# Optimization experiments

Measured on AMD Instinct MI355X. Metric: run time of the kernel, lower is better.

Reference implementation:

```python
import jax, jax.numpy as jnp
import numpy as np

B, N, M, D = 4, 512, 512, 128
H, DOUT = 256, 128

def setup_inputs() -> dict:
    key = jax.random.key(0)
    k = jax.random.split(key, 4)
    X = jax.random.normal(k[0], (B, N, D), dtype=jnp.float32)
    Y = jax.random.normal(k[1], (B, M, D), dtype=jnp.float32)
    W1 = jax.random.normal(k[2], (2 * D, H), dtype=jnp.float32) / np.sqrt(2 * D)
    b1 = jnp.zeros((H,), dtype=jnp.float32)
    W2 = jax.random.normal(k[3], (H, DOUT), dtype=jnp.float32) / np.sqrt(H)
    b2 = jnp.zeros((DOUT,), dtype=jnp.float32)
    return {"X": X, "Y": Y, "W1": W1, "b1": b1, "W2": W2, "b2": b2}

def reference(X, Y, W1, b1, W2, b2):
    # pairs[b,n,m,:] = concat(Y[b,m], X[b,n])  -> [B,N,M,2D]
    n_ = X.shape[1]
    m_ = Y.shape[1]
    Ye = jnp.broadcast_to(Y[:, None, :, :], (X.shape[0], n_, m_, Y.shape[-1]))
    Xe = jnp.broadcast_to(X[:, :, None, :], (X.shape[0], n_, m_, X.shape[-1]))
    pairs = jnp.concatenate([Ye, Xe], axis=-1)
    # pointwise MLP: Linear -> ReLU -> Linear
    hdn = jax.nn.relu(jnp.einsum('bnmd,dh->bnmh', pairs, W1) + b1)
    Z = jnp.einsum('bnmh,ho->bnmo', hdn, W2) + b2
    # pool='sum' over the M (neighbor) dimension
    return jnp.sum(Z, axis=2)  # [B, N, DOUT]
```

## Files before the change

kernel.cpp:

```cpp
#include <hip/hip_runtime.h>

#define BB    4
#define NN    512
#define MM    512
#define DD    128
#define HH    256
#define DOUTC 128

typedef float v2f __attribute__((ext_vector_type(2)));
typedef float v4f __attribute__((ext_vector_type(4)));

__global__ __launch_bounds__(1024) void precompute_ac(
    const float* __restrict__ X, const float* __restrict__ Y,
    const float* __restrict__ W1, const float* __restrict__ b1,
    float* __restrict__ AC)
{
    __shared__ __align__(16) float rows16[16][DD];
    const int bid = blockIdx.x;
    const int t   = threadIdx.x;
    const int isC = bid >> 7;
    const int r0  = (bid & 127) * 16;
    const float* src = isC ? X : Y;

    if (t < 512)
        reinterpret_cast<v4f*>(&rows16[0][0])[t] =
            reinterpret_cast<const v4f*>(src + (size_t)r0 * DD)[t];
    __syncthreads();

    const int hq = t & 63, h0 = hq * 4;
    const int r  = t >> 6;
    const float* wp = W1 + (isC ? DD * HH : 0) + h0;

    v4f acc = (v4f){0.f, 0.f, 0.f, 0.f};
#pragma unroll 2
    for (int dg = 0; dg < DD; dg += 4) {
        const v4f rv = *reinterpret_cast<const v4f*>(&rows16[r][dg]);
        const v4f w0 = *reinterpret_cast<const v4f*>(&wp[(dg + 0) * HH]);
        const v4f w1 = *reinterpret_cast<const v4f*>(&wp[(dg + 1) * HH]);
        const v4f w2 = *reinterpret_cast<const v4f*>(&wp[(dg + 2) * HH]);
        const v4f w3 = *reinterpret_cast<const v4f*>(&wp[(dg + 3) * HH]);
        acc += w0 * rv.x;
        acc += w1 * rv.y;
        acc += w2 * rv.z;
        acc += w3 * rv.w;
    }

    if (isC) acc += *reinterpret_cast<const v4f*>(&b1[h0]);
    *reinterpret_cast<v4f*>(&AC[((size_t)(isC * 2048 + r0 + r)) * HH + h0]) = acc;
}

__global__ __launch_bounds__(1024) void fused_main(
    const float* __restrict__ A, const float* __restrict__ C,
    const float* __restrict__ W2, const float* __restrict__ b2,
    float* __restrict__ out)
{
    __shared__ __align__(16) float Spart[3][8][HH];
    __shared__ __align__(16) float SsatL[4][HH];
    __shared__ __align__(16) float S[8][HH];
    const int bid = blockIdx.x;
    const int b   = bid >> 6;
    const int n0  = (bid & 63) * 8;
    const int t   = threadIdx.x;

    const int hq = t & 63, h0 = hq * 4;
    const int ng = (t >> 6) & 3;
    const int qm = t >> 8;

    const float* Crow = C + ((size_t)(b * NN + n0 + ng * 2)) * HH + h0;
    const v4f c0 = *reinterpret_cast<const v4f*>(&Crow[0]);
    const v4f c1 = *reinterpret_cast<const v4f*>(&Crow[HH]);
    v4f acc0 = (v4f){0.f,0.f,0.f,0.f}, acc1 = acc0, sat = acc0;

    const float* Ab = A + ((size_t)(b * MM + qm * 128)) * HH + h0;
    if (ng == 0) {
#pragma unroll 8
        for (int m = 0; m < 128; ++m) {
            const v4f a = *reinterpret_cast<const v4f*>(&Ab[(size_t)m * HH]);
            sat += a;
            const v4f s0 = a + c0;
            const v4f s1 = a + c1;
            acc0.x += fabsf(s0.x); acc0.y += fabsf(s0.y);
            acc0.z += fabsf(s0.z); acc0.w += fabsf(s0.w);
            acc1.x += fabsf(s1.x); acc1.y += fabsf(s1.y);
            acc1.z += fabsf(s1.z); acc1.w += fabsf(s1.w);
        }
    } else {
#pragma unroll 8
        for (int m = 0; m < 128; ++m) {
            const v4f a = *reinterpret_cast<const v4f*>(&Ab[(size_t)m * HH]);
            const v4f s0 = a + c0;
            const v4f s1 = a + c1;
            acc0.x += fabsf(s0.x); acc0.y += fabsf(s0.y);
            acc0.z += fabsf(s0.z); acc0.w += fabsf(s0.w);
            acc1.x += fabsf(s1.x); acc1.y += fabsf(s1.y);
            acc1.z += fabsf(s1.z); acc1.w += fabsf(s1.w);
        }
    }

    if (qm) {
        *reinterpret_cast<v4f*>(&Spart[qm - 1][ng * 2 + 0][h0]) = acc0;
        *reinterpret_cast<v4f*>(&Spart[qm - 1][ng * 2 + 1][h0]) = acc1;
    }
    if (ng == 0)
        *reinterpret_cast<v4f*>(&SsatL[qm][h0]) = sat;
    __syncthreads();

    if (qm == 0) {
        v4f st = *reinterpret_cast<const v4f*>(&SsatL[0][h0]);
#pragma unroll
        for (int i = 1; i < 4; ++i)
            st += *reinterpret_cast<const v4f*>(&SsatL[i][h0]);
        v4f a0 = acc0, a1 = acc1;
#pragma unroll
        for (int p = 0; p < 3; ++p) {
            a0 += *reinterpret_cast<const v4f*>(&Spart[p][ng * 2 + 0][h0]);
            a1 += *reinterpret_cast<const v4f*>(&Spart[p][ng * 2 + 1][h0]);
        }
        *reinterpret_cast<v4f*>(&S[ng * 2 + 0][h0]) = 0.5f * (st + 512.f * c0 + a0);
        *reinterpret_cast<v4f*>(&S[ng * 2 + 1][h0]) = 0.5f * (st + 512.f * c1 + a1);
    }
    __syncthreads();

    const int o0 = (t & 31) * 4;
    const int r  = (t >> 5) & 7;
    const int kq = t >> 8;
    const int k0 = kq * 64;

    v4f a4 = (v4f){0.f, 0.f, 0.f, 0.f};
    const float* w2p = W2 + o0;
#pragma unroll 4
    for (int k = k0; k < k0 + 64; k += 4) {
        const v4f sv = *reinterpret_cast<const v4f*>(&S[r][k]);
        const v4f wA = *reinterpret_cast<const v4f*>(&w2p[(k + 0) * DOUTC]);
        const v4f wB = *reinterpret_cast<const v4f*>(&w2p[(k + 1) * DOUTC]);
        const v4f wC = *reinterpret_cast<const v4f*>(&w2p[(k + 2) * DOUTC]);
        const v4f wD = *reinterpret_cast<const v4f*>(&w2p[(k + 3) * DOUTC]);
        a4 += wA * sv.x;
        a4 += wB * sv.y;
        a4 += wC * sv.z;
        a4 += wD * sv.w;
    }

    v4f* red = reinterpret_cast<v4f*>(&Spart[0][0][0]);
    if (kq) red[(kq - 1) * 256 + (t & 255)] = a4;
    __syncthreads();
    if (kq == 0) {
#pragma unroll
        for (int p = 0; p < 3; ++p) a4 += red[p * 256 + t];
        a4 += 512.f * (*reinterpret_cast<const v4f*>(&b2[o0]));
        *reinterpret_cast<v4f*>(&out[((size_t)(b * NN + n0 + r)) * DOUTC + o0]) = a4;
    }
}

extern "C" void kernel_launch(void* const* d_in, const int* in_sizes, int n_in,
                              void* d_out, int out_size, void* d_ws, size_t ws_size,
                              hipStream_t stream) {
    const float* X  = (const float*)d_in[0];
    const float* Y  = (const float*)d_in[1];
    const float* W1 = (const float*)d_in[2];
    const float* b1 = (const float*)d_in[3];
    const float* W2 = (const float*)d_in[4];
    const float* b2 = (const float*)d_in[5];
    float* out = (float*)d_out;

    float* AC = (float*)d_ws;
    float* A  = AC;
    float* Cm = AC + 2048 * HH;

    hipLaunchKernelGGL(precompute_ac, dim3(256), dim3(1024), 0, stream,
                       X, Y, W1, b1, AC);
    hipLaunchKernelGGL(fused_main, dim3(256), dim3(1024), 0, stream,
                       A, Cm, W2, b2, out);
}
```

Baseline: 51.26 us.

## Register-tile rows in both kernels and reduce partials with LDS atomics

In precompute_ac, each thread now computes 8 rows over a 16-wide slice of D, so every W1 load is reused across 8 rows. Partial sums are combined with shared-memory float atomics. In fused_main, each wave now handles 32 M rows for all 8 n rows, so each A load is reused 8 times instead of 2, with partial sums again combined through LDS atomics. This cuts global and L2 traffic for A and W1, at the cost of contended LDS atomics, higher register use, and a min-blocks launch-bounds hint that may be unachievable at 1024 threads.

After: 120.5 us. +135.1%, slower.

```diff
diff --git a/kernel.cpp b/kernel.cpp
--- a/kernel.cpp
+++ b/kernel.cpp
@@ -10,12 +10,13 @@
 typedef float v2f __attribute__((ext_vector_type(2)));
 typedef float v4f __attribute__((ext_vector_type(4)));
 
-__global__ __launch_bounds__(1024) void precompute_ac(
+__global__ __launch_bounds__(1024, 4) void precompute_ac(
     const float* __restrict__ X, const float* __restrict__ Y,
     const float* __restrict__ W1, const float* __restrict__ b1,
     float* __restrict__ AC)
 {
-    __shared__ __align__(16) float rows16[16][DD];
+    __shared__ __align__(16) float rows[16][DD];
+    __shared__ __align__(16) float Sacc[16][4][64];
     const int bid = blockIdx.x;
     const int t   = threadIdx.x;
     const int isC = bid >> 7;
@@ -23,101 +24,127 @@
     const float* src = isC ? X : Y;
 
     if (t < 512)
-        reinterpret_cast<v4f*>(&rows16[0][0])[t] =
+        reinterpret_cast<v4f*>(&rows[0][0])[t] =
             reinterpret_cast<const v4f*>(src + (size_t)r0 * DD)[t];
+    reinterpret_cast<v4f*>(&Sacc[0][0][0])[t] = (v4f){0.f, 0.f, 0.f, 0.f};
     __syncthreads();
 
     const int hq = t & 63, h0 = hq * 4;
-    const int r  = t >> 6;
+    const int dq = (t >> 6) & 7;
+    const int d0 = dq * 16;
+    const int rbase = (t >> 9) * 8;
     const float* wp = W1 + (isC ? DD * HH : 0) + h0;
 
-    v4f acc = (v4f){0.f, 0.f, 0.f, 0.f};
-#pragma unroll 2
-    for (int dg = 0; dg < DD; dg += 4) {
-        const v4f rv = *reinterpret_cast<const v4f*>(&rows16[r][dg]);
-        const v4f w0 = *reinterpret_cast<const v4f*>(&wp[(dg + 0) * HH]);
-        const v4f w1 = *reinterpret_cast<const v4f*>(&wp[(dg + 1) * HH]);
-        const v4f w2 = *reinterpret_cast<const v4f*>(&wp[(dg + 2) * HH]);
-        const v4f w3 = *reinterpret_cast<const v4f*>(&wp[(dg + 3) * HH]);
-        acc += w0 * rv.x;
-        acc += w1 * rv.y;
-        acc += w2 * rv.z;
-        acc += w3 * rv.w;
+    v4f acc[8];
+#pragma unroll
+    for (int r = 0; r < 8; ++r) acc[r] = (v4f){0.f, 0.f, 0.f, 0.f};
+
+#pragma unroll
+    for (int dd = 0; dd < 16; dd += 4) {
+        const v4f w0 = *reinterpret_cast<const v4f*>(&wp[(d0 + dd + 0) * HH]);
+        const v4f w1 = *reinterpret_cast<const v4f*>(&wp[(d0 + dd + 1) * HH]);
+        const v4f w2 = *reinterpret_cast<const v4f*>(&wp[(d0 + dd + 2) * HH]);
+        const v4f w3 = *reinterpret_cast<const v4f*>(&wp[(d0 + dd + 3) * HH]);
+#pragma unroll
+        for (int r = 0; r < 8; ++r) {
+            const v4f rv = *reinterpret_cast<const v4f*>(&rows[rbase + r][d0 + dd]);
+            acc[r] += w0 * rv.x;
+            acc[r] += w1 * rv.y;
+            acc[r] += w2 * rv.z;
+            acc[r] += w3 * rv.w;
+        }
     }
 
-    if (isC) acc += *reinterpret_cast<const v4f*>(&b1[h0]);
-    *reinterpret_cast<v4f*>(&AC[((size_t)(isC * 2048 + r0 + r)) * HH + h0]) = acc;
+#pragma unroll
+    for (int r = 0; r < 8; ++r) {
+        atomicAdd(&Sacc[rbase + r][0][hq], acc[r].x);
+        atomicAdd(&Sacc[rbase + r][1][hq], acc[r].y);
+        atomicAdd(&Sacc[rbase + r][2][hq], acc[r].z);
+        atomicAdd(&Sacc[rbase + r][3][hq], acc[r].w);
+    }
+    __syncthreads();
+
+    {
+        const int r = t >> 6;
+        const int l = t & 63;
+        v4f o;
+        o.x = Sacc[r][0][l];
+        o.y = Sacc[r][1][l];
+        o.z = Sacc[r][2][l];
+        o.w = Sacc[r][3][l];
+        if (isC) o += *reinterpret_cast<const v4f*>(&b1[l * 4]);
+        *reinterpret_cast<v4f*>(&AC[((size_t)(isC * 2048 + r0 + r)) * HH + l * 4]) = o;
+    }
 }
 
-__global__ __launch_bounds__(1024) void fused_main(
+__global__ __launch_bounds__(1024, 4) void fused_main(
     const float* __restrict__ A, const float* __restrict__ C,
     const float* __restrict__ W2, const float* __restrict__ b2,
     float* __restrict__ out)
 {
-    __shared__ __align__(16) float Spart[3][8][HH];
-    __shared__ __align__(16) float SsatL[4][HH];
+    __shared__ __align__(16) float Sabs[8][4][64];
+    __shared__ __align__(16) float SATl[4][64];
     __shared__ __align__(16) float S[8][HH];
+    __shared__ __align__(16) v4f red[3 * 256];
     const int bid = blockIdx.x;
     const int b   = bid >> 6;
     const int n0  = (bid & 63) * 8;
     const int t   = threadIdx.x;
 
+    if (t < 512)      reinterpret_cast<v4f*>(&Sabs[0][0][0])[t] = (v4f){0.f,0.f,0.f,0.f};
+    else if (t < 576) reinterpret_cast<v4f*>(&SATl[0][0])[t - 512] = (v4f){0.f,0.f,0.f,0.f};
+    __syncthreads();
+
     const int hq = t & 63, h0 = hq * 4;
-    const int ng = (t >> 6) & 3;
-    const int qm = t >> 8;
+    const int qm = t >> 6;
 
-    const float* Crow = C + ((size_t)(b * NN + n0 + ng * 2)) * HH + h0;
-    const v4f c0 = *reinterpret_cast<const v4f*>(&Crow[0]);
-    const v4f c1 = *reinterpret_cast<const v4f*>(&Crow[HH]);
-    v4f acc0 = (v4f){0.f,0.f,0.f,0.f}, acc1 = acc0, sat = acc0;
+    const float* Cb = C + ((size_t)(b * NN + n0)) * HH + h0;
+    v4f c[8];
+#pragma unroll
+    for (int j = 0; j < 8; ++j)
+        c[j] = *reinterpret_cast<const v4f*>(&Cb[(size_t)j * HH]);
 
-    const float* Ab = A + ((size_t)(b * MM + qm * 128)) * HH + h0;
-    if (ng == 0) {
-#pragma unroll 8
-        for (int m = 0; m < 128; ++m) {
-            const v4f a = *reinterpret_cast<const v4f*>(&Ab[(size_t)m * HH]);
-            sat += a;
-            const v4f s0 = a + c0;
-            const v4f s1 = a + c1;
-            acc0.x += fabsf(s0.x); acc0.y += fabsf(s0.y);
-            acc0.z += fabsf(s0.z); acc0.w += fabsf(s0.w);
-            acc1.x += fabsf(s1.x); acc1.y += fabsf(s1.y);
-            acc1.z += fabsf(s1.z); acc1.w += fabsf(s1.w);
-        }
-    } else {
-#pragma unroll 8
-        for (int m = 0; m < 128; ++m) {
-            const v4f a = *reinterpret_cast<const v4f*>(&Ab[(size_t)m * HH]);
-            const v4f s0 = a + c0;
-            const v4f s1 = a + c1;
-            acc0.x += fabsf(s0.x); acc0.y += fabsf(s0.y);
-            acc0.z += fabsf(s0.z); acc0.w += fabsf(s0.w);
-            acc1.x += fabsf(s1.x); acc1.y += fabsf(s1.y);
-            acc1.z += fabsf(s1.z); acc1.w += fabsf(s1.w);
+    v4f acc[8], sat = (v4f){0.f, 0.f, 0.f, 0.f};
+#pragma unroll
+    for (int j = 0; j < 8; ++j) acc[j] = (v4f){0.f, 0.f, 0.f, 0.f};
+
+    const float* Ab = A + ((size_t)(b * MM + qm * 32)) * HH + h0;
+#pragma unroll 4
+    for (int m = 0; m < 32; ++m) {
+        const v4f a = *reinterpret_cast<const v4f*>(&Ab[(size_t)m * HH]);
+        sat += a;
+#pragma unroll
+        for (int j = 0; j < 8; ++j) {
+            const v4f s = a + c[j];
+            acc[j].x += fabsf(s.x);
+            acc[j].y += fabsf(s.y);
+            acc[j].z += fabsf(s.z);
+            acc[j].w += fabsf(s.w);
         }
     }
 
-    if (qm) {
-        *reinterpret_cast<v4f*>(&Spart[qm - 1][ng * 2 + 0][h0]) = acc0;
-        *reinterpret_cast<v4f*>(&Spart[qm - 1][ng * 2 + 1][h0]) = acc1;
+#pragma unroll
+    for (int j = 0; j < 8; ++j) {
+        atomicAdd(&Sabs[j][0][hq], acc[j].x);
+        atomicAdd(&Sabs[j][1][hq], acc[j].y);
+        atomicAdd(&Sabs[j][2][hq], acc[j].z);
+        atomicAdd(&Sabs[j][3][hq], acc[j].w);
     }
-    if (ng == 0)
-        *reinterpret_cast<v4f*>(&SsatL[qm][h0]) = sat;
+    atomicAdd(&SATl[0][hq], sat.x);
+    atomicAdd(&SATl[1][hq], sat.y);
+    atomicAdd(&SATl[2][hq], sat.z);
+    atomicAdd(&SATl[3][hq], sat.w);
     __syncthreads();
 
-    if (qm == 0) {
-        v4f st = *reinterpret_cast<const v4f*>(&SsatL[0][h0]);
+    {
+        const int r  = t >> 7;
+        const int hh = (t & 127) * 2;
 #pragma unroll
-        for (int i = 1; i < 4; ++i)
-            st += *reinterpret_cast<const v4f*>(&SsatL[i][h0]);
-        v4f a0 = acc0, a1 = acc1;
-#pragma unroll
-        for (int p = 0; p < 3; ++p) {
-            a0 += *reinterpret_cast<const v4f*>(&Spart[p][ng * 2 + 0][h0]);
-            a1 += *reinterpret_cast<const v4f*>(&Spart[p][ng * 2 + 1][h0]);
+        for (int u = 0; u < 2; ++u) {
+            const int h = hh + u;
+            const float cv = C[((size_t)(b * NN + n0 + r)) * HH + h];
+            S[r][h] = 0.5f * (SATl[h & 3][h >> 2] + 512.f * cv + Sabs[r][h & 3][h >> 2]);
         }
-        *reinterpret_cast<v4f*>(&S[ng * 2 + 0][h0]) = 0.5f * (st + 512.f * c0 + a0);
-        *reinterpret_cast<v4f*>(&S[ng * 2 + 1][h0]) = 0.5f * (st + 512.f * c1 + a1);
     }
     __syncthreads();
 
@@ -125,7 +152,6 @@
     const int r  = (t >> 5) & 7;
     const int kq = t >> 8;
     const int k0 = kq * 64;
-
     v4f a4 = (v4f){0.f, 0.f, 0.f, 0.f};
     const float* w2p = W2 + o0;
 #pragma unroll 4
@@ -140,8 +166,6 @@
         a4 += wC * sv.z;
         a4 += wD * sv.w;
     }
-
-    v4f* red = reinterpret_cast<v4f*>(&Spart[0][0][0]);
     if (kq) red[(kq - 1) * 256 + (t & 255)] = a4;
     __syncthreads();
     if (kq == 0) {
```

## Register-block all 8 rows per thread in fused_main and reduce via wave shuffles

Applied to the files above, without the earlier changes.

The main kernel's thread mapping changes so each thread keeps all 8 C rows in registers and streams a strided subset of M. Each loaded A vector is reused 8 times instead of 2, which cuts global/L2 traffic on A by 4x. Partial sums are first reduced across lanes with xor shuffles, then across waves through shared memory. The precompute kernel also gets chunked loops with extra __syncthreads, which serve no apparent purpose and may add barrier overhead. Register pressure rises, since each thread now holds 8 accumulators and 8 C vectors.

Result: slower. 53.86 us (+5.1%).

```diff
diff --git a/kernel.cpp b/kernel.cpp
--- a/kernel.cpp
+++ b/kernel.cpp
@@ -9,6 +9,15 @@
 
 typedef float v2f __attribute__((ext_vector_type(2)));
 typedef float v4f __attribute__((ext_vector_type(4)));
+
+__device__ __forceinline__ v4f shfl_xor4(v4f v, int m) {
+    v4f r;
+    r.x = __shfl_xor(v.x, m, 64);
+    r.y = __shfl_xor(v.y, m, 64);
+    r.z = __shfl_xor(v.z, m, 64);
+    r.w = __shfl_xor(v.w, m, 64);
+    return r;
+}
 
 __global__ __launch_bounds__(1024) void precompute_ac(
     const float* __restrict__ X, const float* __restrict__ Y,
@@ -32,17 +41,22 @@
     const float* wp = W1 + (isC ? DD * HH : 0) + h0;
 
     v4f acc = (v4f){0.f, 0.f, 0.f, 0.f};
+#pragma unroll
+    for (int chunk = 0; chunk < 4; ++chunk) {
+        const int dbase = chunk * 32;
 #pragma unroll 2
-    for (int dg = 0; dg < DD; dg += 4) {
-        const v4f rv = *reinterpret_cast<const v4f*>(&rows16[r][dg]);
-        const v4f w0 = *reinterpret_cast<const v4f*>(&wp[(dg + 0) * HH]);
-        const v4f w1 = *reinterpret_cast<const v4f*>(&wp[(dg + 1) * HH]);
-        const v4f w2 = *reinterpret_cast<const v4f*>(&wp[(dg + 2) * HH]);
-        const v4f w3 = *reinterpret_cast<const v4f*>(&wp[(dg + 3) * HH]);
-        acc += w0 * rv.x;
-        acc += w1 * rv.y;
-        acc += w2 * rv.z;
-        acc += w3 * rv.w;
+        for (int dg = dbase; dg < dbase + 32; dg += 4) {
+            const v4f rv = *reinterpret_cast<const v4f*>(&rows16[r][dg]);
+            const v4f w0 = *reinterpret_cast<const v4f*>(&wp[(dg + 0) * HH]);
+            const v4f w1 = *reinterpret_cast<const v4f*>(&wp[(dg + 1) * HH]);
+            const v4f w2 = *reinterpret_cast<const v4f*>(&wp[(dg + 2) * HH]);
+            const v4f w3 = *reinterpret_cast<const v4f*>(&wp[(dg + 3) * HH]);
+            acc += w0 * rv.x;
+            acc += w1 * rv.y;
+            acc += w2 * rv.z;
+            acc += w3 * rv.w;
+        }
+        if (chunk < 3) __syncthreads();
     }
 
     if (isC) acc += *reinterpret_cast<const v4f*>(&b1[h0]);
@@ -54,70 +68,75 @@
     const float* __restrict__ W2, const float* __restrict__ b2,
     float* __restrict__ out)
 {
-    __shared__ __align__(16) float Spart[3][8][HH];
-    __shared__ __align__(16) float SsatL[4][HH];
+    __shared__ __align__(16) v4f scratch[1536];
+    __shared__ __align__(16) v4f satp[3][4][16];
     __shared__ __align__(16) float S[8][HH];
     const int bid = blockIdx.x;
     const int b   = bid >> 6;
     const int n0  = (bid & 63) * 8;
     const int t   = threadIdx.x;
 
-    const int hq = t & 63, h0 = hq * 4;
-    const int ng = (t >> 6) & 3;
-    const int qm = t >> 8;
+    const int w    = t >> 6;
+    const int l    = t & 63;
+    const int hg   = w & 3;
+    const int qm   = w >> 2;
+    const int hq   = l & 15;
+    const int msub = l >> 4;
+    const int h0   = hg * 64 + hq * 4;
 
-    const float* Crow = C + ((size_t)(b * NN + n0 + ng * 2)) * HH + h0;
-    const v4f c0 = *reinterpret_cast<const v4f*>(&Crow[0]);
-    const v4f c1 = *reinterpret_cast<const v4f*>(&Crow[HH]);
-    v4f acc0 = (v4f){0.f,0.f,0.f,0.f}, acc1 = acc0, sat = acc0;
+    const float* Cb = C + ((size_t)(b * NN + n0)) * HH + h0;
+    v4f c[8];
+#pragma unroll
+    for (int j = 0; j < 8; ++j)
+        c[j] = *reinterpret_cast<const v4f*>(&Cb[(size_t)j * HH]);
 
-    const float* Ab = A + ((size_t)(b * MM + qm * 128)) * HH + h0;
-    if (ng == 0) {
-#pragma unroll 8
-        for (int m = 0; m < 128; ++m) {
-            const v4f a = *reinterpret_cast<const v4f*>(&Ab[(size_t)m * HH]);
-            sat += a;
-            const v4f s0 = a + c0;
-            const v4f s1 = a + c1;
-            acc0.x += fabsf(s0.x); acc0.y += fabsf(s0.y);
-            acc0.z += fabsf(s0.z); acc0.w += fabsf(s0.w);
-            acc1.x += fabsf(s1.x); acc1.y += fabsf(s1.y);
-            acc1.z += fabsf(s1.z); acc1.w += fabsf(s1.w);
-        }
-    } else {
-#pragma unroll 8
-        for (int m = 0; m < 128; ++m) {
-            const v4f a = *reinterpret_cast<const v4f*>(&Ab[(size_t)m * HH]);
-            const v4f s0 = a + c0;
-            const v4f s1 = a + c1;
-            acc0.x += fabsf(s0.x); acc0.y += fabsf(s0.y);
-            acc0.z += fabsf(s0.z); acc0.w += fabsf(s0.w);
-            acc1.x += fabsf(s1.x); acc1.y += fabsf(s1.y);
-            acc1.z += fabsf(s1.z); acc1.w += fabsf(s1.w);
+    v4f acc[8], sat = (v4f){0.f, 0.f, 0.f, 0.f};
+#pragma unroll
+    for (int j = 0; j < 8; ++j) acc[j] = (v4f){0.f, 0.f, 0.f, 0.f};
+
+    const float* Ab = A + ((size_t)(b * MM + qm * 128 + msub)) * HH + h0;
+#pragma unroll 4
+    for (int i = 0; i < 32; ++i) {
+        const v4f a = *reinterpret_cast<const v4f*>(&Ab[(size_t)i * 4 * HH]);
+        sat += a;
+#pragma unroll
+        for (int j = 0; j < 8; ++j) {
+            const v4f s = a + c[j];
+            acc[j].x += fabsf(s.x);
+            acc[j].y += fabsf(s.y);
+            acc[j].z += fabsf(s.z);
+            acc[j].w += fabsf(s.w);
         }
     }
 
-    if (qm) {
-        *reinterpret_cast<v4f*>(&Spart[qm - 1][ng * 2 + 0][h0]) = acc0;
-        *reinterpret_cast<v4f*>(&Spart[qm - 1][ng * 2 + 1][h0]) = acc1;
+#pragma unroll
+    for (int mask = 16; mask <= 32; mask <<= 1) {
+#pragma unroll
+        for (int j = 0; j < 8; ++j) acc[j] += shfl_xor4(acc[j], mask);
+        sat += shfl_xor4(sat, mask);
     }
-    if (ng == 0)
-        *reinterpret_cast<v4f*>(&SsatL[qm][h0]) = sat;
+
+    if (qm > 0 && l < 16) {
+#pragma unroll
+        for (int j = 0; j < 8; ++j)
+            scratch[(((qm - 1) * 4 + hg) * 8 + j) * 16 + l] = acc[j];
+        satp[qm - 1][hg][l] = sat;
+    }
     __syncthreads();
 
-    if (qm == 0) {
-        v4f st = *reinterpret_cast<const v4f*>(&SsatL[0][h0]);
-#pragma unroll
-        for (int i = 1; i < 4; ++i)
-            st += *reinterpret_cast<const v4f*>(&SsatL[i][h0]);
-        v4f a0 = acc0, a1 = acc1;
+    if (qm == 0 && l < 16) {
 #pragma unroll
         for (int p = 0; p < 3; ++p) {
-            a0 += *reinterpret_cast<const v4f*>(&Spart[p][ng * 2 + 0][h0]);
-            a1 += *reinterpret_cast<const v4f*>(&Spart[p][ng * 2 + 1][h0]);
+#pragma unroll
+            for (int j = 0; j < 8; ++j)
+                acc[j] += scratch[((p * 4 + hg) * 8 + j) * 16 + l];
+            sat += satp[p][hg][l];
         }
-        *reinterpret_cast<v4f*>(&S[ng * 2 + 0][h0]) = 0.5f * (st + 512.f * c0 + a0);
-        *reinterpret_cast<v4f*>(&S[ng * 2 + 1][h0]) = 0.5f * (st + 512.f * c1 + a1);
+#pragma unroll
+        for (int j = 0; j < 8; ++j) {
+            const v4f sv = 0.5f * (sat + 512.f * c[j] + acc[j]);
+            *reinterpret_cast<v4f*>(&S[j][h0]) = sv;
+        }
     }
     __syncthreads();
 
@@ -125,7 +144,6 @@
     const int r  = (t >> 5) & 7;
     const int kq = t >> 8;
     const int k0 = kq * 64;
-
     v4f a4 = (v4f){0.f, 0.f, 0.f, 0.f};
     const float* w2p = W2 + o0;
 #pragma unroll 4
@@ -140,13 +158,11 @@
         a4 += wC * sv.z;
         a4 += wD * sv.w;
     }
-
-    v4f* red = reinterpret_cast<v4f*>(&Spart[0][0][0]);
-    if (kq) red[(kq - 1) * 256 + (t & 255)] = a4;
+    if (kq) scratch[(kq - 1) * 256 + (t & 255)] = a4;
     __syncthreads();
     if (kq == 0) {
 #pragma unroll
-        for (int p = 0; p < 3; ++p) a4 += red[p * 256 + t];
+        for (int p = 0; p < 3; ++p) a4 += scratch[p * 256 + t];
         a4 += 512.f * (*reinterpret_cast<const v4f*>(&b2[o0]));
         *reinterpret_cast<v4f*>(&out[((size_t)(b * NN + n0 + r)) * DOUTC + o0]) = a4;
     }
```
